# Kernel optimization log

Hardware: AMD Instinct MI355X
Metric: run time of the kernel (lower is better)

## Reference

```python
import jax, jax.numpy as jnp
import numpy as np

N = 50000       # nodes
E = 600000      # edges
F_IN = 500      # num_feature
H = 64          # hidden_dim (ODE state = 2*H)
C = 40          # num_class
T = 1.0         # integration time
STEPS = 4       # RK4 steps (16 ODE function evals)


def setup_inputs() -> dict:
    key = jax.random.key(0)
    ks = jax.random.split(key, 7)
    x = jax.random.normal(ks[0], (N, F_IN), dtype=jnp.float32)
    edge_src = jax.random.randint(ks[1], (E,), 0, N, dtype=jnp.int32)
    edge_dst = jax.random.randint(ks[2], (E,), 0, N, dtype=jnp.int32)
    edge_w = jax.random.uniform(ks[3], (E,), dtype=jnp.float32)
    m1_w = jax.random.normal(ks[4], (F_IN, H), dtype=jnp.float32) / np.sqrt(F_IN).astype(np.float32)
    m1_b = jnp.zeros((H,), jnp.float32)
    alpha_train = jnp.ones((N,), jnp.float32)  # alpha * ones(N) with alpha=1.0
    m2_w = jax.random.normal(ks[5], (H, C), dtype=jnp.float32) / np.sqrt(H).astype(np.float32)
    m2_b = jnp.zeros((C,), jnp.float32)
    return dict(x=x, edge_w=edge_w, m1_w=m1_w, m1_b=m1_b,
                alpha_train=alpha_train, m2_w=m2_w, m2_b=m2_b,
                edge_src=edge_src, edge_dst=edge_dst)


def spmm(edge_src, edge_dst, edge_w, z):
    # A @ z where A[i,j] = sum of edge_w over edges (src=i, dst=j)
    msg = edge_w[:, None] * z[edge_dst]           # [E, 2H]
    return jax.ops.segment_sum(msg, edge_src, num_segments=N)


def reference(x, edge_w, m1_w, m1_b, alpha_train, m2_w, m2_b, edge_src, edge_dst):
    # Encoder (dropout is identity in eval mode)
    h = x @ m1_w + m1_b                           # [N, H]
    h = jnp.concatenate([h, jnp.zeros_like(h)], axis=1)  # [N, 2H]
    x0 = jax.lax.stop_gradient(h)                 # x0 = x.clone().detach()
    alph = jax.nn.sigmoid(alpha_train)[:, None]   # [N, 1]

    def f(z):  # ODE RHS: sigmoid(alpha)*0.5*(A z - z) + x0
        az = spmm(edge_src, edge_dst, edge_w, z)
        return alph * 0.5 * (az - z) + x0

    dt = jnp.float32(T / STEPS)

    def step(z, _):
        k1 = f(z)
        k2 = f(z + 0.5 * dt * k1)
        k3 = f(z + 0.5 * dt * k2)
        k4 = f(z + dt * k3)
        return z + (dt / 6.0) * (k1 + 2.0 * k2 + 2.0 * k3 + k4), None

    z, _ = jax.lax.scan(step, h, None, length=STEPS)
    z = jax.nn.relu(z[:, :H])                     # first half of state
    return z @ m2_w + m2_b                        # [N, C]
```

## Files before the change

### kernel.cpp

```cpp
#include <hip/hip_runtime.h>
#include <hip/hip_fp16.h>

#define N_NODES 50000
#define N_EDGES 600000
#define F_IN    500
#define H_DIM   64
#define C_OUT   40
#define STEPS   4
#define NB_SCAN ((N_NODES + 255) / 256)
#define KTILES  16

using half8 = __attribute__((ext_vector_type(8))) _Float16;
using f32x4 = __attribute__((ext_vector_type(4))) float;

__global__ __launch_bounds__(256) void bfrag_kernel(
    const float* __restrict__ W, __half* __restrict__ bfrag)
{
    int t = blockIdx.x * 256 + threadIdx.x;
    if (t >= KTILES * 4 * 64) return;
    int lane = t & 63;
    int c    = (t >> 6) & 3;
    int kt   = t >> 8;
    int col  = c * 16 + (lane & 15);
    int kb   = kt * 32 + (lane >> 4) * 8;
    union { uint4 u; __half h[8]; } v;
    #pragma unroll
    for (int j = 0; j < 8; ++j) {
        int k = kb + j;
        v.h[j] = (k < F_IN) ? __float2half(W[(size_t)k * H_DIM + col]) : __half(0.f);
    }
    *reinterpret_cast<uint4*>(bfrag + (size_t)t * 8) = v.u;
}

__global__ __launch_bounds__(256) void encoder_kernel(
    const float* __restrict__ x, const __half* __restrict__ bfrag,
    const float* __restrict__ b, __half* __restrict__ x0H,
    __half* __restrict__ zH)
{
    __shared__ f32x4 red[3][64][4];

    int wave = threadIdx.x >> 6;
    int lane = threadIdx.x & 63;
    int rowl = lane & 15;
    int kg   = lane >> 4;
    int r0   = blockIdx.x * 16;

    int gr = r0 + rowl; if (gr >= N_NODES) gr = N_NODES - 1;
    const float* xrow = x + (size_t)gr * F_IN;
    const uint4* bf = reinterpret_cast<const uint4*>(bfrag);

    int ktb = wave * 4;

    float4 xv[8];
    #pragma unroll
    for (int ki = 0; ki < 4; ++ki) {
        int k0 = (ktb + ki) * 32 + kg * 8;
        xv[2 * ki]     = make_float4(0.f, 0.f, 0.f, 0.f);
        xv[2 * ki + 1] = make_float4(0.f, 0.f, 0.f, 0.f);
        if (k0 + 4 <= F_IN) xv[2 * ki]     = *reinterpret_cast<const float4*>(xrow + k0);
        if (k0 + 8 <= F_IN) xv[2 * ki + 1] = *reinterpret_cast<const float4*>(xrow + k0 + 4);
    }

    f32x4 acc[4];
    #pragma unroll
    for (int c = 0; c < 4; ++c) acc[c] = (f32x4){0.f, 0.f, 0.f, 0.f};

    #pragma unroll
    for (int ki = 0; ki < 4; ++ki) {
        int kt = ktb + ki;
        float4 xa = xv[2 * ki], xb = xv[2 * ki + 1];
        half8 a;
        a[0] = (_Float16)xa.x; a[1] = (_Float16)xa.y;
        a[2] = (_Float16)xa.z; a[3] = (_Float16)xa.w;
        a[4] = (_Float16)xb.x; a[5] = (_Float16)xb.y;
        a[6] = (_Float16)xb.z; a[7] = (_Float16)xb.w;
        #pragma unroll
        for (int c = 0; c < 4; ++c) {
            union { uint4 u; half8 h; } bv;
            bv.u = bf[(size_t)(kt * 4 + c) * 64 + lane];
            acc[c] = __builtin_amdgcn_mfma_f32_16x16x32_f16(a, bv.h, acc[c], 0, 0, 0);
        }
    }

    if (wave > 0) {
        #pragma unroll
        for (int c = 0; c < 4; ++c) red[wave - 1][lane][c] = acc[c];
    }
    __syncthreads();
    if (wave == 0) {
        #pragma unroll
        for (int w = 0; w < 3; ++w)
            #pragma unroll
            for (int c = 0; c < 4; ++c) {
                f32x4 r = red[w][lane][c];
                acc[c][0] += r[0]; acc[c][1] += r[1];
                acc[c][2] += r[2]; acc[c][3] += r[3];
            }
        #pragma unroll
        for (int c = 0; c < 4; ++c) {
            int col = c * 16 + rowl;
            float bias = b[col];
            #pragma unroll
            for (int r = 0; r < 4; ++r) {
                int grow = r0 + kg * 4 + r;
                if (grow < N_NODES) {
                    float v = acc[c][r] + bias;
                    size_t idx = (size_t)grow * H_DIM + col;
                    __half hv = __float2half(v);
                    zH[idx]  = hv;
                    x0H[idx] = hv;
                }
            }
        }
    }
}

__global__ void hist_kernel(const int* __restrict__ src, int* __restrict__ counts)
{
    int e = blockIdx.x * 256 + threadIdx.x;
    if (e < N_EDGES) atomicAdd(&counts[src[e]], 1);
}

__global__ __launch_bounds__(256) void scanA_kernel(
    const int* __restrict__ counts, int* __restrict__ blockSums)
{
    __shared__ int red[256];
    int i = blockIdx.x * 256 + threadIdx.x;
    red[threadIdx.x] = (i < N_NODES) ? counts[i] : 0;
    __syncthreads();
    #pragma unroll
    for (int s = 128; s > 0; s >>= 1) {
        if (threadIdx.x < s) red[threadIdx.x] += red[threadIdx.x + s];
        __syncthreads();
    }
    if (threadIdx.x == 0) blockSums[blockIdx.x] = red[0];
}

__global__ __launch_bounds__(256) void scanB_kernel(
    const int* __restrict__ blockSums, int* __restrict__ blockBases)
{
    __shared__ int s[256];
    int tid = threadIdx.x;
    int v = (tid < NB_SCAN) ? blockSums[tid] : 0;
    s[tid] = v;
    __syncthreads();
    #pragma unroll
    for (int d = 1; d < 256; d <<= 1) {
        int t = (tid >= d) ? s[tid - d] : 0;
        __syncthreads();
        s[tid] += t;
        __syncthreads();
    }
    if (tid < NB_SCAN) blockBases[tid] = s[tid] - v;
}

__global__ __launch_bounds__(256) void scanC_kernel(
    const int* __restrict__ counts, const int* __restrict__ blockBases,
    int* __restrict__ off, int* __restrict__ cursor)
{
    __shared__ int s[256];
    int tid = threadIdx.x;
    int i = blockIdx.x * 256 + tid;
    int v = (i < N_NODES) ? counts[i] : 0;
    s[tid] = v;
    __syncthreads();
    #pragma unroll
    for (int d = 1; d < 256; d <<= 1) {
        int t = (tid >= d) ? s[tid - d] : 0;
        __syncthreads();
        s[tid] += t;
        __syncthreads();
    }
    if (i < N_NODES) {
        int excl = blockBases[blockIdx.x] + s[tid] - v;
        off[i] = excl;
        cursor[i] = excl;
        if (i == N_NODES - 1) off[N_NODES] = excl + v;
    }
}

__global__ void scatter_kernel(const int* __restrict__ src, const int* __restrict__ dst,
                               const float* __restrict__ w,
                               int* __restrict__ cursor, int2* __restrict__ epack)
{
    int e = blockIdx.x * 256 + threadIdx.x;
    if (e < N_EDGES) {
        int s = src[e];
        int p = atomicAdd(&cursor[s], 1);
        epack[p] = make_int2(dst[e] << 7, __float_as_int(w[e]));
    }
}

template<int STAGE>
__global__ __launch_bounds__(256) void stage_kernel(
    const int* __restrict__ off, const int2* __restrict__ epack,
    const __half* __restrict__ zsH, const __half* __restrict__ zH,
    const __half* __restrict__ x0H, const float* __restrict__ alpha,
    __half* __restrict__ accH, __half* __restrict__ outH, float cnext)
{
    int node = blockIdx.x * 32 + (threadIdx.x >> 3);
    if (node >= N_NODES) return;
    int cb = (threadIdx.x & 7) << 4;
    int c  = cb >> 1;

    int jb = off[node], je = off[node + 1];
    const char* rdB = reinterpret_cast<const char*>(zsH);

    union H4 { uint4 u; __half2 h[4]; };

    float azA[8], azB[8];
    #pragma unroll
    for (int i = 0; i < 8; ++i) { azA[i] = 0.f; azB[i] = 0.f; }

#define ACC8(dst, V, W)                                                    \
    {                                                                      \
        float2 f0 = __half22float2((V).h[0]);                              \
        float2 f1 = __half22float2((V).h[1]);                              \
        float2 f2 = __half22float2((V).h[2]);                              \
        float2 f3 = __half22float2((V).h[3]);                              \
        dst[0] = fmaf(W, f0.x, dst[0]); dst[1] = fmaf(W, f0.y, dst[1]);    \
        dst[2] = fmaf(W, f1.x, dst[2]); dst[3] = fmaf(W, f1.y, dst[3]);    \
        dst[4] = fmaf(W, f2.x, dst[4]); dst[5] = fmaf(W, f2.y, dst[5]);    \
        dst[6] = fmaf(W, f3.x, dst[6]); dst[7] = fmaf(W, f3.y, dst[7]);    \
    }

    int j = jb;
    for (; j + 3 < je; j += 4) {
        int2 e0 = epack[j];
        int2 e1 = epack[j + 1];
        int2 e2 = epack[j + 2];
        int2 e3 = epack[j + 3];
        H4 v0, v1, v2, v3;
        v0.u = *reinterpret_cast<const uint4*>(rdB + (size_t)(unsigned)e0.x + cb);
        v1.u = *reinterpret_cast<const uint4*>(rdB + (size_t)(unsigned)e1.x + cb);
        v2.u = *reinterpret_cast<const uint4*>(rdB + (size_t)(unsigned)e2.x + cb);
        v3.u = *reinterpret_cast<const uint4*>(rdB + (size_t)(unsigned)e3.x + cb);
        float w0 = __int_as_float(e0.y), w1 = __int_as_float(e1.y);
        float w2 = __int_as_float(e2.y), w3 = __int_as_float(e3.y);
        ACC8(azA, v0, w0);
        ACC8(azB, v1, w1);
        ACC8(azA, v2, w2);
        ACC8(azB, v3, w3);
    }
    for (; j < je; ++j) {
        int2 e0 = epack[j];
        H4 v0;
        v0.u = *reinterpret_cast<const uint4*>(rdB + (size_t)(unsigned)e0.x + cb);
        float w0 = __int_as_float(e0.y);
        ACC8(azA, v0, w0);
    }
#undef ACC8

    float az[8];
    #pragma unroll
    for (int i = 0; i < 8; ++i) az[i] = azA[i] + azB[i];

    size_t idx = (size_t)node * H_DIM + c;
    H4 sr; sr.u = *reinterpret_cast<const uint4*>(zsH + idx);
    float s[8];
    {
        float2 f0 = __half22float2(sr.h[0]), f1 = __half22float2(sr.h[1]);
        float2 f2 = __half22float2(sr.h[2]), f3 = __half22float2(sr.h[3]);
        s[0] = f0.x; s[1] = f0.y; s[2] = f1.x; s[3] = f1.y;
        s[4] = f2.x; s[5] = f2.y; s[6] = f3.x; s[7] = f3.y;
    }
    H4 xr; xr.u = *reinterpret_cast<const uint4*>(x0H + idx);
    float xv[8];
    {
        float2 f0 = __half22float2(xr.h[0]), f1 = __half22float2(xr.h[1]);
        float2 f2 = __half22float2(xr.h[2]), f3 = __half22float2(xr.h[3]);
        xv[0] = f0.x; xv[1] = f0.y; xv[2] = f1.x; xv[3] = f1.y;
        xv[4] = f2.x; xv[5] = f2.y; xv[6] = f3.x; xv[7] = f3.y;
    }
    float a = 0.5f / (1.f + __expf(-alpha[node]));

    float k[8];
    #pragma unroll
    for (int i = 0; i < 8; ++i) k[i] = fmaf(a, az[i] - s[i], xv[i]);

    float o[8];
    if constexpr (STAGE == 0) {
        H4 aw;
        aw.h[0] = __float22half2_rn(make_float2(k[0], k[1]));
        aw.h[1] = __float22half2_rn(make_float2(k[2], k[3]));
        aw.h[2] = __float22half2_rn(make_float2(k[4], k[5]));
        aw.h[3] = __float22half2_rn(make_float2(k[6], k[7]));
        *reinterpret_cast<uint4*>(accH + idx) = aw.u;
        #pragma unroll
        for (int i = 0; i < 8; ++i) o[i] = fmaf(cnext, k[i], s[i]);
    } else if constexpr (STAGE == 1 || STAGE == 2) {
        H4 ar; ar.u = *reinterpret_cast<const uint4*>(accH + idx);
        float av[8];
        {
            float2 f0 = __half22float2(ar.h[0]), f1 = __half22float2(ar.h[1]);
            float2 f2 = __half22float2(ar.h[2]), f3 = __half22float2(ar.h[3]);
            av[0] = f0.x; av[1] = f0.y; av[2] = f1.x; av[3] = f1.y;
            av[4] = f2.x; av[5] = f2.y; av[6] = f3.x; av[7] = f3.y;
        }
        #pragma unroll
        for (int i = 0; i < 8; ++i) av[i] = fmaf(2.f, k[i], av[i]);
        H4 aw;
        aw.h[0] = __float22half2_rn(make_float2(av[0], av[1]));
        aw.h[1] = __float22half2_rn(make_float2(av[2], av[3]));
        aw.h[2] = __float22half2_rn(make_float2(av[4], av[5]));
        aw.h[3] = __float22half2_rn(make_float2(av[6], av[7]));
        *reinterpret_cast<uint4*>(accH + idx) = aw.u;
        H4 br; br.u = *reinterpret_cast<const uint4*>(zH + idx);
        float bv[8];
        {
            float2 f0 = __half22float2(br.h[0]), f1 = __half22float2(br.h[1]);
            float2 f2 = __half22float2(br.h[2]), f3 = __half22float2(br.h[3]);
            bv[0] = f0.x; bv[1] = f0.y; bv[2] = f1.x; bv[3] = f1.y;
            bv[4] = f2.x; bv[5] = f2.y; bv[6] = f3.x; bv[7] = f3.y;
        }
        #pragma unroll
        for (int i = 0; i < 8; ++i) o[i] = fmaf(cnext, k[i], bv[i]);
    } else {
        H4 ar; ar.u = *reinterpret_cast<const uint4*>(accH + idx);
        float av[8];
        {
            float2 f0 = __half22float2(ar.h[0]), f1 = __half22float2(ar.h[1]);
            float2 f2 = __half22float2(ar.h[2]), f3 = __half22float2(ar.h[3]);
            av[0] = f0.x; av[1] = f0.y; av[2] = f1.x; av[3] = f1.y;
            av[4] = f2.x; av[5] = f2.y; av[6] = f3.x; av[7] = f3.y;
        }
        H4 br; br.u = *reinterpret_cast<const uint4*>(zH + idx);
        float bv[8];
        {
            float2 f0 = __half22float2(br.h[0]), f1 = __half22float2(br.h[1]);
            float2 f2 = __half22float2(br.h[2]), f3 = __half22float2(br.h[3]);
            bv[0] = f0.x; bv[1] = f0.y; bv[2] = f1.x; bv[3] = f1.y;
            bv[4] = f2.x; bv[5] = f2.y; bv[6] = f3.x; bv[7] = f3.y;
        }
        #pragma unroll
        for (int i = 0; i < 8; ++i) o[i] = fmaf(cnext, av[i] + k[i], bv[i]);
    }
    H4 sv;
    sv.h[0] = __float22half2_rn(make_float2(o[0], o[1]));
    sv.h[1] = __float22half2_rn(make_float2(o[2], o[3]));
    sv.h[2] = __float22half2_rn(make_float2(o[4], o[5]));
    sv.h[3] = __float22half2_rn(make_float2(o[6], o[7]));
    *reinterpret_cast<uint4*>(outH + idx) = sv.u;
}

__global__ __launch_bounds__(256) void decoder_kernel(
    const __half* __restrict__ zH, const float* __restrict__ W2,
    const float* __restrict__ b2, float* __restrict__ out)
{
    __shared__ float zsm[4][H_DIM];
    int lane = threadIdx.x & 63;
    int w    = threadIdx.x >> 6;
    int node = blockIdx.x * 4 + w;
    int ld   = node >= N_NODES ? N_NODES - 1 : node;
    float zv = __half2float(zH[(size_t)ld * H_DIM + lane]);
    zsm[w][lane] = zv > 0.f ? zv : 0.f;
    __syncthreads();
    if (node < N_NODES && lane < C_OUT) {
        float acc = b2[lane];
        #pragma unroll
        for (int k = 0; k < H_DIM; ++k)
            acc = fmaf(zsm[w][k], W2[k * C_OUT + lane], acc);
        out[(size_t)node * C_OUT + lane] = acc;
    }
}

extern "C" void kernel_launch(void* const* d_in, const int* in_sizes, int n_in,
                              void* d_out, int out_size, void* d_ws, size_t ws_size,
                              hipStream_t stream)
{
    const float* x     = (const float*)d_in[0];
    const float* ew    = (const float*)d_in[1];
    const float* m1w   = (const float*)d_in[2];
    const float* m1b   = (const float*)d_in[3];
    const float* alpha = (const float*)d_in[4];
    const float* m2w   = (const float*)d_in[5];
    const float* m2b   = (const float*)d_in[6];
    const int*   esrc  = (const int*)d_in[7];
    const int*   edst  = (const int*)d_in[8];
    float* out = (float*)d_out;

    char* ws = (char*)d_ws;
    size_t o = 0;
    auto alloc = [&](size_t bytes) -> void* {
        void* p = ws + o;
        o = (o + bytes + 255) & ~(size_t)255;
        return p;
    };
    __half* x0H    = (__half*)alloc((size_t)N_NODES * H_DIM * 2);
    __half* zH     = (__half*)alloc((size_t)N_NODES * H_DIM * 2);
    __half* ztAH   = (__half*)alloc((size_t)N_NODES * H_DIM * 2);
    __half* ztBH   = (__half*)alloc((size_t)N_NODES * H_DIM * 2);
    __half* accH   = (__half*)alloc((size_t)N_NODES * H_DIM * 2);
    __half* bfrag  = (__half*)alloc((size_t)KTILES * 4 * 64 * 8 * 2);
    int*    counts = (int*)alloc((size_t)N_NODES * 4);
    int*    off    = (int*)alloc((size_t)(N_NODES + 1) * 4);
    int*    cursor = (int*)alloc((size_t)N_NODES * 4);
    int*    bsums  = (int*)alloc((size_t)NB_SCAN * 4);
    int*    bbases = (int*)alloc((size_t)NB_SCAN * 4);
    int2*   epack  = (int2*)alloc((size_t)N_EDGES * 8);

    hipMemsetAsync(counts, 0, (size_t)N_NODES * 4, stream);
    hist_kernel<<<(N_EDGES + 255) / 256, 256, 0, stream>>>(esrc, counts);
    scanA_kernel<<<NB_SCAN, 256, 0, stream>>>(counts, bsums);
    scanB_kernel<<<1, 256, 0, stream>>>(bsums, bbases);
    scanC_kernel<<<NB_SCAN, 256, 0, stream>>>(counts, bbases, off, cursor);
    scatter_kernel<<<(N_EDGES + 255) / 256, 256, 0, stream>>>(esrc, edst, ew, cursor, epack);

    bfrag_kernel<<<(KTILES * 4 * 64 + 255) / 256, 256, 0, stream>>>(m1w, bfrag);
    encoder_kernel<<<(N_NODES + 15) / 16, 256, 0, stream>>>(x, bfrag, m1b, x0H, zH);

    const float dt = 1.0f / STEPS;
    int sgrid = (N_NODES + 31) / 32;
    for (int step = 0; step < STEPS; ++step) {
        stage_kernel<0><<<sgrid, 256, 0, stream>>>(off, epack, zH,   zH, x0H, alpha, accH, ztAH, 0.5f * dt);
        stage_kernel<1><<<sgrid, 256, 0, stream>>>(off, epack, ztAH, zH, x0H, alpha, accH, ztBH, 0.5f * dt);
        stage_kernel<2><<<sgrid, 256, 0, stream>>>(off, epack, ztBH, zH, x0H, alpha, accH, ztAH, dt);
        stage_kernel<3><<<sgrid, 256, 0, stream>>>(off, epack, ztAH, zH, x0H, alpha, accH, zH,   dt / 6.0f);
    }

    decoder_kernel<<<(N_NODES + 3) / 4, 256, 0, stream>>>(zH, m2w, m2b, out);
}
```

Before: 389.1 us.

## Stage encoder rows through LDS and pack edge entries into 32 bits

The encoder now loads each 16-row tile of x into shared memory with coalesced float4 reads, then feeds the MFMA fragments from LDS. It also writes the fp16 output through an LDS staging tile so each lane stores 16-byte vectors instead of scattered 2-byte stores. Separately, each edge entry shrinks from an int2 (scaled dst offset plus fp32 weight) to one 32-bit word holding a 16-bit dst index and an fp16 weight, halving edge-list traffic in the 16 stage kernels. The weight loses precision to fp16, and the 16-bit index only works because node ids stay below 65536.

```diff
diff --git a/kernel.cpp b/kernel.cpp
--- a/kernel.cpp
+++ b/kernel.cpp
@@ -9,6 +9,7 @@
 #define STEPS   4
 #define NB_SCAN ((N_NODES + 255) / 256)
 #define KTILES  16
+#define XS_COLS 516
 
 using half8 = __attribute__((ext_vector_type(8))) _Float16;
 using f32x4 = __attribute__((ext_vector_type(4))) float;
@@ -37,38 +38,45 @@
     const float* __restrict__ b, __half* __restrict__ x0H,
     __half* __restrict__ zH)
 {
+    __shared__ __align__(16) float xs[16][XS_COLS];
     __shared__ f32x4 red[3][64][4];
-
-    int wave = threadIdx.x >> 6;
-    int lane = threadIdx.x & 63;
+    __shared__ float outs[16][68];
+
+    int t    = threadIdx.x;
+    int wave = t >> 6;
+    int lane = t & 63;
+    int r0   = blockIdx.x * 16;
+
+    #pragma unroll
+    for (int i = 0; i < 8; ++i) {
+        int c = i * 64 + lane;
+        if (c < 500) {
+            int row = c / 125;
+            int cc  = c - row * 125;
+            int grow = r0 + wave * 4 + row;
+            if (grow >= N_NODES) grow = N_NODES - 1;
+            float4 v = *reinterpret_cast<const float4*>(x + (size_t)grow * F_IN + cc * 4);
+            *reinterpret_cast<float4*>(&xs[wave * 4 + row][cc * 4]) = v;
+        }
+    }
+    xs[t >> 4][500 + (t & 15)] = 0.f;
+    __syncthreads();
+
     int rowl = lane & 15;
     int kg   = lane >> 4;
-    int r0   = blockIdx.x * 16;
-
-    int gr = r0 + rowl; if (gr >= N_NODES) gr = N_NODES - 1;
-    const float* xrow = x + (size_t)gr * F_IN;
     const uint4* bf = reinterpret_cast<const uint4*>(bfrag);
 
+    f32x4 acc[4];
+    #pragma unroll
+    for (int c = 0; c < 4; ++c) acc[c] = (f32x4){0.f, 0.f, 0.f, 0.f};
+
     int ktb = wave * 4;
-
-    float4 xv[8];
-    #pragma unroll
-    for (int ki = 0; ki < 4; ++ki) {
-        int k0 = (ktb + ki) * 32 + kg * 8;
-        xv[2 * ki]     = make_float4(0.f, 0.f, 0.f, 0.f);
-        xv[2 * ki + 1] = make_float4(0.f, 0.f, 0.f, 0.f);
-        if (k0 + 4 <= F_IN) xv[2 * ki]     = *reinterpret_cast<const float4*>(xrow + k0);
-        if (k0 + 8 <= F_IN) xv[2 * ki + 1] = *reinterpret_cast<const float4*>(xrow + k0 + 4);
-    }
-
-    f32x4 acc[4];
-    #pragma unroll
-    for (int c = 0; c < 4; ++c) acc[c] = (f32x4){0.f, 0.f, 0.f, 0.f};
-
     #pragma unroll
     for (int ki = 0; ki < 4; ++ki) {
         int kt = ktb + ki;
-        float4 xa = xv[2 * ki], xb = xv[2 * ki + 1];
+        int k0 = kt * 32 + kg * 8;
+        float4 xa = *reinterpret_cast<const float4*>(&xs[rowl][k0]);
+        float4 xb = *reinterpret_cast<const float4*>(&xs[rowl][k0 + 4]);
         half8 a;
         a[0] = (_Float16)xa.x; a[1] = (_Float16)xa.y;
         a[2] = (_Float16)xa.z; a[3] = (_Float16)xa.w;
@@ -101,16 +109,21 @@
             int col = c * 16 + rowl;
             float bias = b[col];
             #pragma unroll
-            for (int r = 0; r < 4; ++r) {
-                int grow = r0 + kg * 4 + r;
-                if (grow < N_NODES) {
-                    float v = acc[c][r] + bias;
-                    size_t idx = (size_t)grow * H_DIM + col;
-                    __half hv = __float2half(v);
-                    zH[idx]  = hv;
-                    x0H[idx] = hv;
-                }
-            }
+            for (int r = 0; r < 4; ++r)
+                outs[kg * 4 + r][col] = acc[c][r] + bias;
+        }
+        int orow = lane >> 2;
+        int ocb  = (lane & 3) * 16;
+        int grow = r0 + orow;
+        if (grow < N_NODES) {
+            union { uint4 u[2]; __half h[16]; } pk;
+            #pragma unroll
+            for (int i = 0; i < 16; ++i) pk.h[i] = __float2half(outs[orow][ocb + i]);
+            size_t idx = (size_t)grow * H_DIM + ocb;
+            *reinterpret_cast<uint4*>(zH  + idx)     = pk.u[0];
+            *reinterpret_cast<uint4*>(zH  + idx + 8) = pk.u[1];
+            *reinterpret_cast<uint4*>(x0H + idx)     = pk.u[0];
+            *reinterpret_cast<uint4*>(x0H + idx + 8) = pk.u[1];
         }
     }
 }
@@ -181,19 +194,20 @@
 
 __global__ void scatter_kernel(const int* __restrict__ src, const int* __restrict__ dst,
                                const float* __restrict__ w,
-                               int* __restrict__ cursor, int2* __restrict__ epack)
+                               int* __restrict__ cursor, unsigned* __restrict__ epack)
 {
     int e = blockIdx.x * 256 + threadIdx.x;
     if (e < N_EDGES) {
         int s = src[e];
         int p = atomicAdd(&cursor[s], 1);
-        epack[p] = make_int2(dst[e] << 7, __float_as_int(w[e]));
+        unsigned wh = (unsigned)__half_as_ushort(__float2half(w[e]));
+        epack[p] = (unsigned)dst[e] | (wh << 16);
     }
 }
 
 template<int STAGE>
 __global__ __launch_bounds__(256) void stage_kernel(
-    const int* __restrict__ off, const int2* __restrict__ epack,
+    const int* __restrict__ off, const unsigned* __restrict__ epack,
     const __half* __restrict__ zsH, const __half* __restrict__ zH,
     const __half* __restrict__ x0H, const float* __restrict__ alpha,
     __half* __restrict__ accH, __half* __restrict__ outH, float cnext)
@@ -207,11 +221,14 @@
     const char* rdB = reinterpret_cast<const char*>(zsH);
 
     union H4 { uint4 u; __half2 h[4]; };
+    union HW { unsigned short us; __half h; };
 
     float azA[8], azB[8];
     #pragma unroll
     for (int i = 0; i < 8; ++i) { azA[i] = 0.f; azB[i] = 0.f; }
 
+#define WOF(E)  ((size_t)((E) & 0xFFFFu) << 7)
+#define WGT(E)  ({ HW hw_; hw_.us = (unsigned short)((E) >> 16); __half2float(hw_.h); })
 #define ACC8(dst, V, W)                                                    \
     {                                                                      \
         float2 f0 = __half22float2((V).h[0]);                              \
@@ -226,30 +243,31 @@
 
     int j = jb;
     for (; j + 3 < je; j += 4) {
-        int2 e0 = epack[j];
-        int2 e1 = epack[j + 1];
-        int2 e2 = epack[j + 2];
-        int2 e3 = epack[j + 3];
+        unsigned e0 = epack[j];
+        unsigned e1 = epack[j + 1];
+        unsigned e2 = epack[j + 2];
+        unsigned e3 = epack[j + 3];
         H4 v0, v1, v2, v3;
-        v0.u = *reinterpret_cast<const uint4*>(rdB + (size_t)(unsigned)e0.x + cb);
-        v1.u = *reinterpret_cast<const uint4*>(rdB + (size_t)(unsigned)e1.x + cb);
-        v2.u = *reinterpret_cast<const uint4*>(rdB + (size_t)(unsigned)e2.x + cb);
-        v3.u = *reinterpret_cast<const uint4*>(rdB + (size_t)(unsigned)e3.x + cb);
-        float w0 = __int_as_float(e0.y), w1 = __int_as_float(e1.y);
-        float w2 = __int_as_float(e2.y), w3 = __int_as_float(e3.y);
+        v0.u = *reinterpret_cast<const uint4*>(rdB + WOF(e0) + cb);
+        v1.u = *reinterpret_cast<const uint4*>(rdB + WOF(e1) + cb);
+        v2.u = *reinterpret_cast<const uint4*>(rdB + WOF(e2) + cb);
+        v3.u = *reinterpret_cast<const uint4*>(rdB + WOF(e3) + cb);
+        float w0 = WGT(e0), w1 = WGT(e1), w2 = WGT(e2), w3 = WGT(e3);
         ACC8(azA, v0, w0);
         ACC8(azB, v1, w1);
         ACC8(azA, v2, w2);
         ACC8(azB, v3, w3);
     }
     for (; j < je; ++j) {
-        int2 e0 = epack[j];
+        unsigned e0 = epack[j];
         H4 v0;
-        v0.u = *reinterpret_cast<const uint4*>(rdB + (size_t)(unsigned)e0.x + cb);
-        float w0 = __int_as_float(e0.y);
+        v0.u = *reinterpret_cast<const uint4*>(rdB + WOF(e0) + cb);
+        float w0 = WGT(e0);
         ACC8(azA, v0, w0);
     }
 #undef ACC8
+#undef WOF
+#undef WGT
 
     float az[8];
     #pragma unroll
@@ -386,18 +404,18 @@
         o = (o + bytes + 255) & ~(size_t)255;
         return p;
     };
-    __half* x0H    = (__half*)alloc((size_t)N_NODES * H_DIM * 2);
-    __half* zH     = (__half*)alloc((size_t)N_NODES * H_DIM * 2);
-    __half* ztAH   = (__half*)alloc((size_t)N_NODES * H_DIM * 2);
-    __half* ztBH   = (__half*)alloc((size_t)N_NODES * H_DIM * 2);
-    __half* accH   = (__half*)alloc((size_t)N_NODES * H_DIM * 2);
-    __half* bfrag  = (__half*)alloc((size_t)KTILES * 4 * 64 * 8 * 2);
-    int*    counts = (int*)alloc((size_t)N_NODES * 4);
-    int*    off    = (int*)alloc((size_t)(N_NODES + 1) * 4);
-    int*    cursor = (int*)alloc((size_t)N_NODES * 4);
-    int*    bsums  = (int*)alloc((size_t)NB_SCAN * 4);
-    int*    bbases = (int*)alloc((size_t)NB_SCAN * 4);
-    int2*   epack  = (int2*)alloc((size_t)N_EDGES * 8);
+    __half*   x0H    = (__half*)alloc((size_t)N_NODES * H_DIM * 2);
+    __half*   zH     = (__half*)alloc((size_t)N_NODES * H_DIM * 2);
+    __half*   ztAH   = (__half*)alloc((size_t)N_NODES * H_DIM * 2);
+    __half*   ztBH   = (__half*)alloc((size_t)N_NODES * H_DIM * 2);
+    __half*   accH   = (__half*)alloc((size_t)N_NODES * H_DIM * 2);
+    __half*   bfrag  = (__half*)alloc((size_t)KTILES * 4 * 64 * 8 * 2);
+    int*      counts = (int*)alloc((size_t)N_NODES * 4);
+    int*      off    = (int*)alloc((size_t)(N_NODES + 1) * 4);
+    int*      cursor = (int*)alloc((size_t)N_NODES * 4);
+    int*      bsums  = (int*)alloc((size_t)NB_SCAN * 4);
+    int*      bbases = (int*)alloc((size_t)NB_SCAN * 4);
+    unsigned* epack  = (unsigned*)alloc((size_t)N_EDGES * 4);
 
     hipMemsetAsync(counts, 0, (size_t)N_NODES * 4, stream);
     hist_kernel<<<(N_EDGES + 255) / 256, 256, 0, stream>>>(esrc, counts);
```

Result: faster. 363.4 us, median of 2 (-6.6%).
